# Kernel tuning notes

Hardware: AMD Instinct MI355X
Metric: run time of the kernel (lower is better)

The kernel has to match this reference:

```python
import jax, jax.numpy as jnp
import numpy as np

NUM_CLASSES = 10
LABEL_SMOOTHING = 0.1
GAMMA = 2.0
TRANSFORM_PENALTY = 0.2
EXACT_MATCH_BONUS = 5.0
CREATIVITY_WEIGHT = 0.15


def setup_inputs() -> dict:
    key = jax.random.key(0)
    k1, k2, k3, k4 = jax.random.split(key, 4)
    B, C, H, W = 512, NUM_CLASSES, 64, 64
    return {
        "pred_output": jax.random.normal(k1, (B, C, H, W), dtype=jnp.float32),
        "targets": jax.random.randint(k2, (B, H, W), 0, NUM_CLASSES, dtype=jnp.int32),
        "inputs": jax.random.randint(k3, (B, H, W), 0, NUM_CLASSES, dtype=jnp.int32),
        "strategic_reasoning": jax.random.normal(k4, (B, 128), dtype=jnp.float32),
    }


def _diversity_bonus(pred_idx):
    # Encode each 2x2 window as a base-10 integer (colors in [0,10) -> code < 10000),
    # then count distinct codes per sample with a presence bitmap (GPU-friendly dedup).
    B, H, W = pred_idx.shape
    codes = (pred_idx[:, :-1, :-1] * 1000 + pred_idx[:, :-1, 1:] * 100
             + pred_idx[:, 1:, :-1] * 10 + pred_idx[:, 1:, 1:])  # [B, H-1, W-1]
    codes = codes.reshape(B, -1)

    def count_unique(c):
        present = jnp.zeros((NUM_CLASSES ** 4,), dtype=jnp.float32).at[c].set(1.0)
        return present.sum()

    n_unique = jax.vmap(count_unique)(codes)  # [B]
    diversity = n_unique / ((H - 1) * (W - 1))
    return diversity.mean() * 0.02


def reference(pred_output, targets, inputs, strategic_reasoning):
    B, C, H, W = pred_output.shape

    # Label smoothing (applied to the one-hot targets; argmax is unchanged,
    # matching the original where CE is taken on the argmax'ed indices).
    targets_oh = jax.nn.one_hot(targets, C, axis=1, dtype=pred_output.dtype)
    smooth_targets = targets_oh * (1.0 - LABEL_SMOOTHING) + LABEL_SMOOTHING / C
    target_idx = jnp.argmax(smooth_targets, axis=1)  # == targets

    # Strategic focal loss
    logp = jax.nn.log_softmax(pred_output, axis=1)  # [B,C,H,W]
    ce = -jnp.take_along_axis(logp, target_idx[:, None, :, :], axis=1)[:, 0]  # [B,H,W]
    pt = jnp.exp(-ce)
    present = jax.nn.one_hot(targets, C, dtype=jnp.float32).max(axis=(1, 2))  # [B,C]
    unique_colors = present.sum(axis=-1)  # [B]
    strategic_weights = jnp.where(unique_colors > 3, 1.2, 1.0)  # [B]
    focal_loss = ((1.0 - pt) ** GAMMA * ce * strategic_weights[:, None, None]).mean()

    # Exact match / IoU stats
    pred_idx = jnp.argmax(pred_output, axis=1)  # [B,H,W]
    eq = (pred_idx == target_idx)
    exact_matches_strict = jnp.all(eq, axis=(1, 2)).astype(jnp.float32)
    intersection = eq.astype(jnp.float32).sum(axis=(1, 2))
    union = H * W
    iou_scores = intersection / union
    combined_matches = 0.2 * exact_matches_strict + 0.8 * iou_scores
    exact_count = combined_matches.sum()
    exact_bonus = jnp.maximum(-combined_matches.mean() * EXACT_MATCH_BONUS, -3.0)

    # Copy penalty
    copy_penalty = jnp.all(pred_idx == inputs, axis=(1, 2)).astype(jnp.float32)
    transform_penalty = copy_penalty.mean() * TRANSFORM_PENALTY

    # Creativity bonus
    creativity_bonus = jax.nn.sigmoid(strategic_reasoning).mean() * CREATIVITY_WEIGHT

    # Pattern diversity bonus
    diversity_bonus = _diversity_bonus(pred_idx)

    # Grid complexity bonus (H > 15 for our shapes)
    grid_size_factor = jnp.minimum(H * W / 900.0, 1.0)
    grid_complexity_bonus = combined_matches.mean() * grid_size_factor * 0.05

    total_loss = (focal_loss + transform_penalty + exact_bonus
                  - creativity_bonus - diversity_bonus - grid_complexity_bonus)
    bad = jnp.isnan(total_loss) | jnp.isinf(total_loss)
    total_loss = jnp.where(bad, jnp.minimum(focal_loss, 10.0), total_loss)

    return (total_loss, focal_loss, transform_penalty, exact_bonus, exact_count,
            combined_matches.sum(), iou_scores.mean(), creativity_bonus,
            diversity_bonus, grid_complexity_bonus)
```

## Files before the change

### kernel.cpp

```cpp
#include <hip/hip_runtime.h>
#include <math.h>

#define B_   512
#define C_   10
#define HW_  4096
#define NT   512
#define NWIN 3969
#define NBMP 313

__device__ __forceinline__ float block_sum(float v, volatile float* sp, int tid) {
#pragma unroll
    for (int off = 32; off > 0; off >>= 1) v += __shfl_down(v, off, 64);
    __syncthreads();
    if ((tid & 63) == 0) sp[tid >> 6] = v;
    __syncthreads();
    float s = 0.f;
    if (tid == 0) {
#pragma unroll
        for (int i = 0; i < NT / 64; ++i) s += sp[i];
    }
    return s;
}

__global__ __launch_bounds__(NT, 4) void loss_main(
    const float* __restrict__ pred, const int* __restrict__ tgt,
    const int* __restrict__ inp, const float* __restrict__ strat,
    float* __restrict__ ws)
{
    const int b   = blockIdx.x;
    const int tid = threadIdx.x;

    __shared__ unsigned char s_pred[HW_];
    __shared__ unsigned int  s_bmp[NBMP];
    __shared__ unsigned char s_col[C_];
    __shared__ float         s_red[NT / 64];

    for (int i = tid; i < NBMP; i += NT) s_bmp[i] = 0u;
    if (tid < C_) s_col[tid] = 0;
    __syncthreads();

    const float* pb = pred + (size_t)b * C_ * HW_;
    const int*   tb = tgt + b * HW_;
    const int*   ib = inp + b * HW_;

    float focal = 0.f;
    int eqc = 0, dfc = 0;

#pragma unroll
    for (int k = 0; k < 2; ++k) {
        const int p = (k * NT + tid) * 4;
        const int4 t4 = *(const int4*)(tb + p);
        const int4 i4 = *(const int4*)(ib + p);
        float x[C_][4];
#pragma unroll
        for (int c = 0; c < C_; ++c) {
            const float4 v = *(const float4*)(pb + c * HW_ + p);
            x[c][0] = v.x; x[c][1] = v.y; x[c][2] = v.z; x[c][3] = v.w;
        }
#pragma unroll
        for (int e = 0; e < 4; ++e) {
            const int t  = (e == 0) ? t4.x : (e == 1) ? t4.y : (e == 2) ? t4.z : t4.w;
            const int iv = (e == 0) ? i4.x : (e == 1) ? i4.y : (e == 2) ? i4.z : i4.w;
            s_col[t] = 1;
            float mx = x[0][e]; int am = 0;
#pragma unroll
            for (int c = 1; c < C_; ++c) {
                if (x[c][e] > mx) { mx = x[c][e]; am = c; }
            }
            float se = 0.f, ext = 0.f, xt = 0.f;
#pragma unroll
            for (int c = 0; c < C_; ++c) {
                const float ee = __expf(x[c][e] - mx);
                se += ee;
                if (c == t) { ext = ee; xt = x[c][e]; }
            }
            const float lse = mx + __logf(se);
            const float ce  = lse - xt;
            const float pt  = ext / se;
            const float om  = 1.f - pt;
            focal += om * om * ce;
            eqc += (am == t);
            dfc += (am != iv);
            s_pred[p + e] = (unsigned char)am;
        }
    }

    float cre = 0.f;
    if (tid < 128) {
        const float sv = strat[b * 128 + tid];
        cre = 1.f / (1.f + __expf(-sv));
    }

    __syncthreads();

    for (int idx = tid; idx < NWIN; idx += NT) {
        const int r = idx / 63;
        const int c = idx - r * 63;
        const int base = r * 64 + c;
        const unsigned code = (unsigned)s_pred[base]      * 1000u
                            + (unsigned)s_pred[base + 1]  * 100u
                            + (unsigned)s_pred[base + 64] * 10u
                            + (unsigned)s_pred[base + 65];
        atomicOr(&s_bmp[code >> 5], 1u << (code & 31u));
    }
    __syncthreads();
    int nu = 0;
    if (tid < NBMP) nu = __popc(s_bmp[tid]);

    const float focal_t = block_sum(focal, s_red, tid);
    const float eq_t    = block_sum((float)eqc, s_red, tid);
    const float df_t    = block_sum((float)dfc, s_red, tid);
    const float nu_t    = block_sum((float)nu, s_red, tid);
    const float cre_t   = block_sum(cre, s_red, tid);

    if (tid == 0) {
        int uc = 0;
#pragma unroll
        for (int c = 0; c < C_; ++c) uc += s_col[c];
        const float w = (uc > 3) ? 1.2f : 1.0f;
        ws[0 * B_ + b] = focal_t * w;
        ws[1 * B_ + b] = eq_t;
        ws[2 * B_ + b] = (eq_t == 4096.f) ? 1.f : 0.f;
        ws[3 * B_ + b] = (df_t == 0.f) ? 1.f : 0.f;
        ws[4 * B_ + b] = nu_t;
        ws[5 * B_ + b] = cre_t;
    }
}

__global__ __launch_bounds__(NT) void loss_final(
    const float* __restrict__ ws, float* __restrict__ out)
{
    const int tid = threadIdx.x;
    __shared__ float s_red[NT / 64];

    const float focal_b = ws[0 * B_ + tid];
    const float inter   = ws[1 * B_ + tid];
    const float strict  = ws[2 * B_ + tid];
    const float copyf   = ws[3 * B_ + tid];
    const float nu      = ws[4 * B_ + tid];
    const float cre     = ws[5 * B_ + tid];

    const float iou  = inter * (1.f / 4096.f);
    const float comb = 0.2f * strict + 0.8f * iou;
    const float divb = nu * (1.f / 3969.f);

    const float focal_s = block_sum(focal_b, s_red, tid);
    const float comb_s  = block_sum(comb, s_red, tid);
    const float iou_s   = block_sum(iou, s_red, tid);
    const float copy_s  = block_sum(copyf, s_red, tid);
    const float div_s   = block_sum(divb, s_red, tid);
    const float cre_s   = block_sum(cre, s_red, tid);

    if (tid == 0) {
        const float focal_loss        = focal_s / (512.f * 4096.f);
        const float comb_mean         = comb_s / 512.f;
        const float exact_count       = comb_s;
        const float exact_bonus       = fmaxf(-comb_mean * 5.f, -3.f);
        const float transform_penalty = (copy_s / 512.f) * 0.2f;
        const float creativity        = (cre_s / (512.f * 128.f)) * 0.15f;
        const float diversity         = (div_s / 512.f) * 0.02f;
        const float gcb               = comb_mean * 0.05f;

        float total = focal_loss + transform_penalty + exact_bonus
                    - creativity - diversity - gcb;
        if (isnan(total) || isinf(total)) total = fminf(focal_loss, 10.f);

        out[0] = total;
        out[1] = focal_loss;
        out[2] = transform_penalty;
        out[3] = exact_bonus;
        out[4] = exact_count;
        out[5] = exact_count;
        out[6] = iou_s / 512.f;
        out[7] = creativity;
        out[8] = diversity;
        out[9] = gcb;
    }
}

extern "C" void kernel_launch(void* const* d_in, const int* in_sizes, int n_in,
                              void* d_out, int out_size, void* d_ws, size_t ws_size,
                              hipStream_t stream)
{
    const float* pred  = (const float*)d_in[0];
    const int*   tgt   = (const int*)d_in[1];
    const int*   inp   = (const int*)d_in[2];
    const float* strat = (const float*)d_in[3];
    float* ws  = (float*)d_ws;
    float* out = (float*)d_out;

    hipLaunchKernelGGL(loss_main, dim3(B_), dim3(NT), 0, stream,
                       pred, tgt, inp, strat, ws);
    hipLaunchKernelGGL(loss_final, dim3(1), dim3(NT), 0, stream, ws, out);
}
```

Before: 32.14 us.

## Use 1024-thread blocks with packed predictions and single-pass wave reductions

The main kernel now runs 1024 threads per sample, one thread per 4 pixels. Each thread loads float2 pairs and packs its argmax bytes into one 32-bit shared word. The window-code pass is restructured so each thread produces four adjacent 2x2 codes from two packed words. The five serial block_sum reductions, each with two barriers, are replaced by xor-shuffle wave sums plus a single shared-memory combine, and the color-presence flag becomes a bitmask OR. This cuts barriers and shared-memory traffic, but raises per-block thread count and register pressure, and launch_bounds(1024,8) may force register spills.

```diff
diff --git a/kernel.cpp b/kernel.cpp
--- a/kernel.cpp
+++ b/kernel.cpp
@@ -1,28 +1,20 @@
 #include <hip/hip_runtime.h>
 #include <math.h>
 
-#define B_   512
-#define C_   10
-#define HW_  4096
-#define NT   512
-#define NWIN 3969
-#define NBMP 313
-
-__device__ __forceinline__ float block_sum(float v, volatile float* sp, int tid) {
-#pragma unroll
-    for (int off = 32; off > 0; off >>= 1) v += __shfl_down(v, off, 64);
-    __syncthreads();
-    if ((tid & 63) == 0) sp[tid >> 6] = v;
-    __syncthreads();
-    float s = 0.f;
-    if (tid == 0) {
-#pragma unroll
-        for (int i = 0; i < NT / 64; ++i) s += sp[i];
-    }
-    return s;
-}
-
-__global__ __launch_bounds__(NT, 4) void loss_main(
+#define B_    512
+#define C_    10
+#define HW_   4096
+#define NTA   1024
+#define NTF   512
+#define NBMP  313
+
+__device__ __forceinline__ float wave_sum_f(float v) {
+#pragma unroll
+    for (int off = 32; off > 0; off >>= 1) v += __shfl_xor(v, off, 64);
+    return v;
+}
+
+__global__ __launch_bounds__(NTA, 8) void loss_main(
     const float* __restrict__ pred, const int* __restrict__ tgt,
     const int* __restrict__ inp, const float* __restrict__ strat,
     float* __restrict__ ws)
@@ -30,60 +22,60 @@
     const int b   = blockIdx.x;
     const int tid = threadIdx.x;
 
-    __shared__ unsigned char s_pred[HW_];
-    __shared__ unsigned int  s_bmp[NBMP];
-    __shared__ unsigned char s_col[C_];
-    __shared__ float         s_red[NT / 64];
-
-    for (int i = tid; i < NBMP; i += NT) s_bmp[i] = 0u;
-    if (tid < C_) s_col[tid] = 0;
-    __syncthreads();
-
-    const float* pb = pred + (size_t)b * C_ * HW_;
-    const int*   tb = tgt + b * HW_;
-    const int*   ib = inp + b * HW_;
+    __shared__ unsigned int s_pred32[HW_ / 4];
+    __shared__ unsigned int s_bmp[NBMP];
+    __shared__ float        s_red[16][5];
+    __shared__ unsigned int s_cmask;
+
+    if (tid < NBMP) s_bmp[tid] = 0u;
+    if (tid == 0) s_cmask = 0u;
+
+    const int p = tid << 2;
+    const float* pb = pred + (size_t)b * (C_ * HW_) + p;
+    const int4 t4 = *(const int4*)(tgt + b * HW_ + p);
 
     float focal = 0.f;
-    int eqc = 0, dfc = 0;
-
-#pragma unroll
-    for (int k = 0; k < 2; ++k) {
-        const int p = (k * NT + tid) * 4;
-        const int4 t4 = *(const int4*)(tb + p);
-        const int4 i4 = *(const int4*)(ib + p);
-        float x[C_][4];
+    unsigned pack = 0u, cmask = 0u;
+    int eqc = 0;
+
+#pragma unroll
+    for (int h = 0; h < 2; ++h) {
+        float x[C_][2];
 #pragma unroll
         for (int c = 0; c < C_; ++c) {
-            const float4 v = *(const float4*)(pb + c * HW_ + p);
-            x[c][0] = v.x; x[c][1] = v.y; x[c][2] = v.z; x[c][3] = v.w;
-        }
-#pragma unroll
-        for (int e = 0; e < 4; ++e) {
-            const int t  = (e == 0) ? t4.x : (e == 1) ? t4.y : (e == 2) ? t4.z : t4.w;
-            const int iv = (e == 0) ? i4.x : (e == 1) ? i4.y : (e == 2) ? i4.z : i4.w;
-            s_col[t] = 1;
-            float mx = x[0][e]; int am = 0;
-#pragma unroll
-            for (int c = 1; c < C_; ++c) {
-                if (x[c][e] > mx) { mx = x[c][e]; am = c; }
+            const float2 v = *(const float2*)(pb + c * HW_ + h * 2);
+            x[c][0] = v.x; x[c][1] = v.y;
+        }
+#pragma unroll
+        for (int e2 = 0; e2 < 2; ++e2) {
+            const int e = h * 2 + e2;
+            const int t = (e == 0) ? t4.x : (e == 1) ? t4.y : (e == 2) ? t4.z : t4.w;
+            cmask |= 1u << t;
+            float mx = x[0][e2]; int am = 0;
+#pragma unroll
+            for (int c = 1; c < C_; ++c)
+                if (x[c][e2] > mx) { mx = x[c][e2]; am = c; }
+            float se = 0.f, xt = 0.f;
+#pragma unroll
+            for (int c = 0; c < C_; ++c) {
+                se += __expf(x[c][e2] - mx);
+                if (c == t) xt = x[c][e2];
             }
-            float se = 0.f, ext = 0.f, xt = 0.f;
-#pragma unroll
-            for (int c = 0; c < C_; ++c) {
-                const float ee = __expf(x[c][e] - mx);
-                se += ee;
-                if (c == t) { ext = ee; xt = x[c][e]; }
-            }
-            const float lse = mx + __logf(se);
-            const float ce  = lse - xt;
-            const float pt  = ext / se;
-            const float om  = 1.f - pt;
+            const float ce = (mx + __logf(se)) - xt;
+            const float pt = __expf(-ce);
+            const float om = 1.f - pt;
             focal += om * om * ce;
             eqc += (am == t);
-            dfc += (am != iv);
-            s_pred[p + e] = (unsigned char)am;
-        }
-    }
+            pack |= (unsigned)am << (8 * e);
+        }
+    }
+    s_pred32[tid] = pack;
+
+    const int4 i4 = *(const int4*)(inp + b * HW_ + p);
+    const int dfc = ((int)((pack      ) & 0xffu) != i4.x)
+                  + ((int)((pack >>  8) & 0xffu) != i4.y)
+                  + ((int)((pack >> 16) & 0xffu) != i4.z)
+                  + ((int)((pack >> 24) & 0xffu) != i4.w);
 
     float cre = 0.f;
     if (tid < 128) {
@@ -93,45 +85,91 @@
 
     __syncthreads();
 
-    for (int idx = tid; idx < NWIN; idx += NT) {
-        const int r = idx / 63;
-        const int c = idx - r * 63;
-        const int base = r * 64 + c;
-        const unsigned code = (unsigned)s_pred[base]      * 1000u
-                            + (unsigned)s_pred[base + 1]  * 100u
-                            + (unsigned)s_pred[base + 64] * 10u
-                            + (unsigned)s_pred[base + 65];
-        atomicOr(&s_bmp[code >> 5], 1u << (code & 31u));
-    }
-    __syncthreads();
-    int nu = 0;
-    if (tid < NBMP) nu = __popc(s_bmp[tid]);
-
-    const float focal_t = block_sum(focal, s_red, tid);
-    const float eq_t    = block_sum((float)eqc, s_red, tid);
-    const float df_t    = block_sum((float)dfc, s_red, tid);
-    const float nu_t    = block_sum((float)nu, s_red, tid);
-    const float cre_t   = block_sum(cre, s_red, tid);
-
+    {
+        const int r  = tid >> 4;
+        const int c4 = (tid & 15) << 2;
+        if (r < 63) {
+            const int di = tid;
+            const unsigned w0 = s_pred32[di];
+            const unsigned w1 = s_pred32[di + 16];
+            const unsigned n0 = (c4 < 60) ? s_pred32[di + 1]  : 0u;
+            const unsigned n1 = (c4 < 60) ? s_pred32[di + 17] : 0u;
+            const unsigned a0 =  w0        & 0xffu, a1 = (w0 >>  8) & 0xffu,
+                           a2 = (w0 >> 16) & 0xffu, a3 = (w0 >> 24) & 0xffu,
+                           a4 =  n0        & 0xffu;
+            const unsigned b0 =  w1        & 0xffu, b1 = (w1 >>  8) & 0xffu,
+                           b2 = (w1 >> 16) & 0xffu, b3 = (w1 >> 24) & 0xffu,
+                           b4 =  n1        & 0xffu;
+            unsigned code;
+            code = a0 * 1000u + a1 * 100u + b0 * 10u + b1;
+            atomicOr(&s_bmp[code >> 5], 1u << (code & 31u));
+            code = a1 * 1000u + a2 * 100u + b1 * 10u + b2;
+            atomicOr(&s_bmp[code >> 5], 1u << (code & 31u));
+            code = a2 * 1000u + a3 * 100u + b2 * 10u + b3;
+            atomicOr(&s_bmp[code >> 5], 1u << (code & 31u));
+            if (c4 < 60) {
+                code = a3 * 1000u + a4 * 100u + b3 * 10u + b4;
+                atomicOr(&s_bmp[code >> 5], 1u << (code & 31u));
+            }
+        }
+    }
+    __syncthreads();
+
+    const int nu = (tid < NBMP) ? __popc(s_bmp[tid]) : 0;
+
+    const float rf = wave_sum_f(focal);
+    const float re = wave_sum_f((float)eqc);
+    const float rd = wave_sum_f((float)dfc);
+    const float rc = wave_sum_f(cre);
+    const float rn = wave_sum_f((float)nu);
+#pragma unroll
+    for (int off = 32; off > 0; off >>= 1)
+        cmask |= (unsigned)__shfl_xor((int)cmask, off, 64);
+
+    const int wv = tid >> 6;
+    if ((tid & 63) == 0) {
+        s_red[wv][0] = rf; s_red[wv][1] = re; s_red[wv][2] = rd;
+        s_red[wv][3] = rc; s_red[wv][4] = rn;
+        atomicOr(&s_cmask, cmask);
+    }
+    __syncthreads();
     if (tid == 0) {
-        int uc = 0;
-#pragma unroll
-        for (int c = 0; c < C_; ++c) uc += s_col[c];
-        const float w = (uc > 3) ? 1.2f : 1.0f;
-        ws[0 * B_ + b] = focal_t * w;
-        ws[1 * B_ + b] = eq_t;
-        ws[2 * B_ + b] = (eq_t == 4096.f) ? 1.f : 0.f;
-        ws[3 * B_ + b] = (df_t == 0.f) ? 1.f : 0.f;
-        ws[4 * B_ + b] = nu_t;
-        ws[5 * B_ + b] = cre_t;
-    }
-}
-
-__global__ __launch_bounds__(NT) void loss_final(
+        float F = 0.f, E = 0.f, D = 0.f, CR = 0.f, NU = 0.f;
+#pragma unroll
+        for (int i = 0; i < 16; ++i) {
+            F += s_red[i][0]; E += s_red[i][1]; D += s_red[i][2];
+            CR += s_red[i][3]; NU += s_red[i][4];
+        }
+        const int uc = __popc(s_cmask);
+        const float sw = (uc > 3) ? 1.2f : 1.0f;
+        ws[0 * B_ + b] = F * sw;
+        ws[1 * B_ + b] = E;
+        ws[2 * B_ + b] = (E == 4096.f) ? 1.f : 0.f;
+        ws[3 * B_ + b] = (D == 0.f) ? 1.f : 0.f;
+        ws[4 * B_ + b] = NU;
+        ws[5 * B_ + b] = CR;
+    }
+}
+
+__device__ __forceinline__ float block_sum(float v, volatile float* sp, int tid) {
+#pragma unroll
+    for (int off = 32; off > 0; off >>= 1) v += __shfl_down(v, off, 64);
+    __syncthreads();
+    if ((tid & 63) == 0) sp[tid >> 6] = v;
+    __syncthreads();
+    float s = 0.f;
+    if (tid == 0) {
+#pragma unroll
+        for (int i = 0; i < NTF / 64; ++i) s += sp[i];
+    }
+    return s;
+}
+
+__global__ __launch_bounds__(NTF) void loss_final(
     const float* __restrict__ ws, float* __restrict__ out)
 {
     const int tid = threadIdx.x;
-    __shared__ float s_red[NT / 64];
+    __shared__ float s_red[NTF / 64];
 
     const float focal_b = ws[0 * B_ + tid];
     const float inter   = ws[1 * B_ + tid];
@@ -189,7 +227,7 @@
     float* ws  = (float*)d_ws;
     float* out = (float*)d_out;
 
-    hipLaunchKernelGGL(loss_main, dim3(B_), dim3(NT), 0, stream,
+    hipLaunchKernelGGL(loss_main, dim3(B_), dim3(NTA), 0, stream,
                        pred, tgt, inp, strat, ws);
-    hipLaunchKernelGGL(loss_final, dim3(1), dim3(NT), 0, stream, ws, out);
-}
+    hipLaunchKernelGGL(loss_final, dim3(1), dim3(NTF), 0, stream, ws, out);
+}
```

After: 33.41 us. 1.04x slower.
